# Kernel tuning notes

Hardware: AMD Instinct MI355X
Metric: run time of the kernel (lower is better)

The kernel has to match this reference:

```python
import jax, jax.numpy as jnp
import numpy as np

B, T, N, IN_DIM = 32, 12, 1024, 1
HID, EMB, K, HOR, OUT = 64, 16, 2, 12, 1


def setup_inputs() -> dict:
    key = jax.random.key(0)
    ks = jax.random.split(key, 12)
    s = 0.1
    return {
        "x": jax.random.normal(ks[0], (B, T, N, IN_DIM), jnp.float32),
        "E": jax.random.normal(ks[1], (N, EMB), jnp.float32),
        # layer 1: gate (z,r) and candidate pools; in = IN_DIM + HID
        "Wg1": jax.random.normal(ks[2], (EMB, K, IN_DIM + HID, 2 * HID), jnp.float32) * s,
        "bg1": jax.random.normal(ks[3], (EMB, 2 * HID), jnp.float32) * s,
        "Wc1": jax.random.normal(ks[4], (EMB, K, IN_DIM + HID, HID), jnp.float32) * s,
        "bc1": jax.random.normal(ks[5], (EMB, HID), jnp.float32) * s,
        # layer 2: in = HID + HID
        "Wg2": jax.random.normal(ks[6], (EMB, K, 2 * HID, 2 * HID), jnp.float32) * s,
        "bg2": jax.random.normal(ks[7], (EMB, 2 * HID), jnp.float32) * s,
        "Wc2": jax.random.normal(ks[8], (EMB, K, 2 * HID, HID), jnp.float32) * s,
        "bc2": jax.random.normal(ks[9], (EMB, HID), jnp.float32) * s,
        # Conv2d(1, HOR*OUT, kernel=(1, HID)) == per-node linear HID -> HOR*OUT
        "Wout": jax.random.normal(ks[10], (HOR * OUT, HID), jnp.float32) * s,
        "bout": jnp.zeros((HOR * OUT,), jnp.float32),
    }


def _supports(E):
    # adaptive adjacency from node embeddings + Chebyshev polynomial set
    A = jax.nn.softmax(jax.nn.relu(E @ E.T), axis=1)  # [N, N]
    sup = [jnp.eye(E.shape[0], dtype=E.dtype), A]
    for _ in range(K - 2):
        sup.append(2.0 * (A @ sup[-1]) - sup[-2])
    return jnp.stack(sup[:K])  # [K, N, N]


def _gconv(x, sup, E, Wp, bp):
    # x: [B, N, Ci]; per-node weights generated from embeddings
    xg = jnp.einsum('knm,bmc->bnkc', sup, x)          # [B, N, K, Ci]
    W = jnp.einsum('nd,dkio->nkio', E, Wp)            # [N, K, Ci, Co]
    b = E @ bp                                        # [N, Co]
    return jnp.einsum('bnki,nkio->bno', xg, W) + b


def _layer(xs, sup, E, Wg, bg, Wc, bc):
    # xs: [T, B, N, Ci]; adaptive graph-conv GRU scanned over time
    hid = Wc.shape[-1]

    def step(h, x_t):
        zr = jax.nn.sigmoid(_gconv(jnp.concatenate([x_t, h], -1), sup, E, Wg, bg))
        z, r = jnp.split(zr, 2, axis=-1)
        hc = jnp.tanh(_gconv(jnp.concatenate([x_t, z * h], -1), sup, E, Wc, bc))
        h_new = r * h + (1.0 - r) * hc
        return h_new, h_new

    h0 = jnp.zeros((xs.shape[1], xs.shape[2], hid), xs.dtype)
    _, hs = jax.lax.scan(step, h0, xs)
    return hs  # [T, B, N, hid]


def reference(x, E, Wg1, bg1, Wc1, bc1, Wg2, bg2, Wc2, bc2, Wout, bout):
    sup = _supports(E)
    xs = jnp.swapaxes(x, 0, 1)                        # [T, B, N, in]
    h1 = _layer(xs, sup, E, Wg1, bg1, Wc1, bc1)       # [T, B, N, HID]
    h2 = _layer(h1, sup, E, Wg2, bg2, Wc2, bc2)       # [T, B, N, HID]
    h_last = h2[-1]                                   # [B, N, HID]
    out = jnp.einsum('bnh,oh->bno', h_last, Wout) + bout  # [B, N, HOR*OUT]
    out = jnp.transpose(out, (0, 2, 1)).reshape(x.shape[0], HOR, OUT, N)
    return jnp.transpose(out, (0, 1, 3, 2))           # [B, HOR, N, OUT]
```

## Files before the change

kernel.cpp:

```cpp
#include <hip/hip_runtime.h>
#include <math.h>

#define NN 1024
#define BB 32
#define TTT 12
#define HH 64
#define DD 16

__device__ __forceinline__ float dot4f(const float4 v, const float* __restrict__ wv) {
    return v.x * wv[0] + v.y * wv[1] + v.z * wv[2] + v.w * wv[3];
}

__device__ __forceinline__ float sigmoidf_(float x) { return 1.0f / (1.0f + expf(-x)); }

__global__ __launch_bounds__(256) void compute_A_kernel(const float* __restrict__ E,
                                                        float* __restrict__ A) {
    int n = blockIdx.x;
    int tid = threadIdx.x;
    __shared__ float en[DD];
    __shared__ float red[256];
    if (tid < DD) en[tid] = E[n * DD + tid];
    __syncthreads();
    float s[4];
    float lmax = 0.0f;
    #pragma unroll
    for (int it = 0; it < 4; ++it) {
        int m = tid + it * 256;
        float acc = 0.0f;
        #pragma unroll
        for (int d = 0; d < DD; ++d) acc += en[d] * E[m * DD + d];
        acc = fmaxf(acc, 0.0f);
        s[it] = acc;
        lmax = fmaxf(lmax, acc);
    }
    red[tid] = lmax; __syncthreads();
    for (int st = 128; st > 0; st >>= 1) {
        if (tid < st) red[tid] = fmaxf(red[tid], red[tid + st]);
        __syncthreads();
    }
    float mx = red[0];
    __syncthreads();
    float lsum = 0.0f;
    #pragma unroll
    for (int it = 0; it < 4; ++it) { s[it] = expf(s[it] - mx); lsum += s[it]; }
    red[tid] = lsum; __syncthreads();
    for (int st = 128; st > 0; st >>= 1) {
        if (tid < st) red[tid] += red[tid + st];
        __syncthreads();
    }
    float inv = 1.0f / red[0];
    #pragma unroll
    for (int it = 0; it < 4; ++it) {
        int m = tid + it * 256;
        A[n * NN + m] = s[it] * inv;
    }
}

__global__ __launch_bounds__(256) void gen_w_f32_kernel(const float* __restrict__ E,
                                                        const float* __restrict__ Wp,
                                                        float* __restrict__ out,
                                                        int rowlen, int total) {
    int idx = blockIdx.x * 256 + threadIdx.x;
    if (idx >= total) return;
    int n = idx / rowlen;
    int j = idx - n * rowlen;
    const float* e = E + n * DD;
    float acc = 0.0f;
    #pragma unroll
    for (int d = 0; d < DD; ++d) acc += e[d] * Wp[d * rowlen + j];
    out[idx] = acc;
}

__global__ __launch_bounds__(256) void transpose_x_kernel(const float* __restrict__ x,
                                                          float* __restrict__ xTm) {
    int idx = blockIdx.x * 256 + threadIdx.x;
    int m = idx / (TTT * BB);
    int tb = idx - m * (TTT * BB);
    int t = tb >> 5;
    int b = tb & 31;
    xTm[idx] = x[(b * TTT + t) * NN + m];
}

__global__ __launch_bounds__(256) void diffuse_gemm(const float* __restrict__ A,
                                                    const float* __restrict__ S,
                                                    float* __restrict__ C, int cols) {
    __shared__ alignas(16) float As[16][68];
    __shared__ alignas(16) float Bs[16][64];
    const int tid = threadIdx.x;
    const int tx = tid & 15, ty = tid >> 4;
    const int rowbase = blockIdx.y * 64, colbase = blockIdx.x * 64;
    const int kl = tid & 15, r0 = (tid >> 4) * 4;
    const int ml = tid >> 6, cl = tid & 63;
    float pa[4], pb[4];
    #pragma unroll
    for (int r = 0; r < 4; ++r)
        pa[r] = A[(size_t)(rowbase + r0 + r) * NN + kl];
    #pragma unroll
    for (int mm = 0; mm < 4; ++mm)
        pb[mm] = S[(size_t)(ml + mm * 4) * cols + colbase + cl];
    float acc[4][4] = {};
    for (int kt = 0; kt < NN; kt += 16) {
        #pragma unroll
        for (int r = 0; r < 4; ++r) As[kl][r0 + r] = pa[r];
        #pragma unroll
        for (int mm = 0; mm < 4; ++mm) Bs[ml + mm * 4][cl] = pb[mm];
        __syncthreads();
        int kn = kt + 16;
        if (kn < NN) {
            #pragma unroll
            for (int r = 0; r < 4; ++r)
                pa[r] = A[(size_t)(rowbase + r0 + r) * NN + kn + kl];
            #pragma unroll
            for (int mm = 0; mm < 4; ++mm)
                pb[mm] = S[(size_t)(kn + ml + mm * 4) * cols + colbase + cl];
        }
        #pragma unroll
        for (int kk = 0; kk < 16; ++kk) {
            float4 a = *(const float4*)&As[kk][ty * 4];
            float4 b = *(const float4*)&Bs[kk][tx * 4];
            acc[0][0] += a.x * b.x; acc[0][1] += a.x * b.y; acc[0][2] += a.x * b.z; acc[0][3] += a.x * b.w;
            acc[1][0] += a.y * b.x; acc[1][1] += a.y * b.y; acc[1][2] += a.y * b.z; acc[1][3] += a.y * b.w;
            acc[2][0] += a.z * b.x; acc[2][1] += a.z * b.y; acc[2][2] += a.z * b.z; acc[2][3] += a.z * b.w;
            acc[3][0] += a.w * b.x; acc[3][1] += a.w * b.y; acc[3][2] += a.w * b.z; acc[3][3] += a.w * b.w;
        }
        __syncthreads();
    }
    #pragma unroll
    for (int i = 0; i < 4; ++i) {
        float4 v = make_float4(acc[i][0], acc[i][1], acc[i][2], acc[i][3]);
        *(float4*)&C[(size_t)(rowbase + ty * 4 + i) * cols + colbase + tx * 4] = v;
    }
}


__global__ __launch_bounds__(256) void l1_gate_fused(int t,
        const float* __restrict__ xTm, const float* __restrict__ AxA,
        const float* __restrict__ h1, const float* __restrict__ Ah1,
        const float* __restrict__ E, const float4* __restrict__ Wp4,
        const float* __restrict__ Bg,
        float* __restrict__ zh, float* __restrict__ rb) {
    int n = blockIdx.x, tid = threadIdx.x;
    __shared__ float en[DD];
    __shared__ alignas(16) float Wl[65 * 128];
    __shared__ alignas(16) float S0[BB * HH];
    __shared__ alignas(16) float S1[BB * HH];
    __shared__ float sx[BB], sax[BB];
    if (tid < DD) en[tid] = E[n * DD + tid];
    for (int i = tid; i < BB * HH; i += 256) {
        S0[i] = h1[(size_t)n * (BB * HH) + i];
        S1[i] = Ah1[(size_t)n * (BB * HH) + i];
    }
    if (tid < BB) sx[tid] = xTm[n * (TTT * BB) + t * BB + tid];
    else if (tid < 2 * BB) sax[tid - BB] = AxA[n * (TTT * BB) + t * BB + (tid - BB)];
    __syncthreads();
    const int o = tid & 63, bq = tid >> 6;
    float accA[8], accB[8];
    float biasA = Bg[n * 128 + o], biasB = Bg[n * 128 + 64 + o];
    #pragma unroll
    for (int j = 0; j < 8; ++j) { accA[j] = biasA; accB[j] = biasB; }
    for (int k = 0; k < 2; ++k) {
        for (int idx = tid; idx < 2080; idx += 256) {
            float4 a = make_float4(0.f, 0.f, 0.f, 0.f);
            #pragma unroll
            for (int d = 0; d < DD; ++d) {
                float ed = en[d];
                float4 w = Wp4[(size_t)d * 4160 + k * 2080 + idx];
                a.x += ed * w.x; a.y += ed * w.y; a.z += ed * w.z; a.w += ed * w.w;
            }
            *(float4*)&Wl[idx * 4] = a;
        }
        __syncthreads();
        const float* S = (k == 0) ? S0 : S1;
        float wxa = Wl[o], wxb = Wl[64 + o];
        #pragma unroll
        for (int j = 0; j < 8; ++j) {
            int b = bq * 8 + j;
            float xv = (k == 0) ? sx[b] : sax[b];
            accA[j] += xv * wxa; accB[j] += xv * wxb;
        }
        for (int i = 0; i < HH; i += 4) {
            float wa[4], wb[4];
            #pragma unroll
            for (int q = 0; q < 4; ++q) {
                int row = (1 + i + q) * 128;
                wa[q] = Wl[row + o]; wb[q] = Wl[row + 64 + o];
            }
            #pragma unroll
            for (int j = 0; j < 8; ++j) {
                int b = bq * 8 + j;
                float4 sv = *(const float4*)&S[b * HH + i];
                accA[j] += dot4f(sv, wa); accB[j] += dot4f(sv, wb);
            }
        }
        __syncthreads();
    }
    #pragma unroll
    for (int j = 0; j < 8; ++j) {
        int b = bq * 8 + j;
        float z = sigmoidf_(accA[j]);
        float r = sigmoidf_(accB[j]);
        zh[(size_t)n * (BB * HH) + b * HH + o] = z * S0[b * HH + o];
        rb[(size_t)n * (BB * HH) + b * HH + o] = r;
    }
}

__global__ __launch_bounds__(256) void l1_cand_fused(int t,
        const float* __restrict__ xTm, const float* __restrict__ AxA,
        const float* __restrict__ zhb, const float* __restrict__ azh,
        const float* __restrict__ E, const float4* __restrict__ Wp4,
        const float* __restrict__ Bc,
        const float* __restrict__ rb, float* __restrict__ h1) {
    int n = blockIdx.x, tid = threadIdx.x;
    __shared__ float en[DD];
    __shared__ alignas(16) float Wl[65 * 64];
    __shared__ alignas(16) float S0[BB * HH];
    __shared__ alignas(16) float S1[BB * HH];
    __shared__ float sx[BB], sax[BB];
    if (tid < DD) en[tid] = E[n * DD + tid];
    for (int i = tid; i < BB * HH; i += 256) {
        S0[i] = zhb[(size_t)n * (BB * HH) + i];
        S1[i] = azh[(size_t)n * (BB * HH) + i];
    }
    if (tid < BB) sx[tid] = xTm[n * (TTT * BB) + t * BB + tid];
    else if (tid < 2 * BB) sax[tid - BB] = AxA[n * (TTT * BB) + t * BB + (tid - BB)];
    __syncthreads();
    const int o = tid & 63, bq = tid >> 6;
    float acc[8];
    float bias = Bc[n * 64 + o];
    #pragma unroll
    for (int j = 0; j < 8; ++j) acc[j] = bias;
    for (int k = 0; k < 2; ++k) {
        for (int idx = tid; idx < 1040; idx += 256) {
            float4 a = make_float4(0.f, 0.f, 0.f, 0.f);
            #pragma unroll
            for (int d = 0; d < DD; ++d) {
                float ed = en[d];
                float4 w = Wp4[(size_t)d * 2080 + k * 1040 + idx];
                a.x += ed * w.x; a.y += ed * w.y; a.z += ed * w.z; a.w += ed * w.w;
            }
            *(float4*)&Wl[idx * 4] = a;
        }
        __syncthreads();
        const float* S = (k == 0) ? S0 : S1;
        float wx = Wl[o];
        #pragma unroll
        for (int j = 0; j < 8; ++j) {
            int b = bq * 8 + j;
            float xv = (k == 0) ? sx[b] : sax[b];
            acc[j] += xv * wx;
        }
        for (int i = 0; i < HH; i += 4) {
            float wa[4];
            #pragma unroll
            for (int q = 0; q < 4; ++q) wa[q] = Wl[(1 + i + q) * 64 + o];
            #pragma unroll
            for (int j = 0; j < 8; ++j) {
                int b = bq * 8 + j;
                float4 sv = *(const float4*)&S[b * HH + i];
                acc[j] += dot4f(sv, wa);
            }
        }
        __syncthreads();
    }
    #pragma unroll
    for (int j = 0; j < 8; ++j) {
        int b = bq * 8 + j;
        size_t idx = (size_t)n * (BB * HH) + b * HH + o;
        float hc = tanhf(acc[j]);
        float r = rb[idx];
        float hold = h1[idx];
        h1[idx] = r * hold + (1.0f - r) * hc;
    }
}

__global__ __launch_bounds__(256) void l2_gate_fused(
        const float* __restrict__ h1, const float* __restrict__ Ah1,
        const float* __restrict__ h2, const float* __restrict__ Ah2,
        const float* __restrict__ E, const float4* __restrict__ Wp4,
        const float* __restrict__ Bg,
        float* __restrict__ zh, float* __restrict__ rb) {
    int n = blockIdx.x, tid = threadIdx.x;
    __shared__ float en[DD];
    __shared__ alignas(16) float Wl[64 * 128];
    __shared__ alignas(16) float Sl[4][BB * HH];
    if (tid < DD) en[tid] = E[n * DD + tid];
    for (int i = tid; i < BB * HH; i += 256) {
        size_t base = (size_t)n * (BB * HH) + i;
        Sl[0][i] = h1[base]; Sl[1][i] = h2[base];
        Sl[2][i] = Ah1[base]; Sl[3][i] = Ah2[base];
    }
    __syncthreads();
    const int o = tid & 63, bq = tid >> 6;
    float accA[8], accB[8];
    float biasA = Bg[n * 128 + o], biasB = Bg[n * 128 + 64 + o];
    #pragma unroll
    for (int j = 0; j < 8; ++j) { accA[j] = biasA; accB[j] = biasB; }
    for (int p = 0; p < 4; ++p) {
        int k = p >> 1, half = p & 1;
        for (int idx = tid; idx < 2048; idx += 256) {
            float4 a = make_float4(0.f, 0.f, 0.f, 0.f);
            #pragma unroll
            for (int d = 0; d < DD; ++d) {
                float ed = en[d];
                float4 w = Wp4[(size_t)d * 8192 + k * 4096 + half * 2048 + idx];
                a.x += ed * w.x; a.y += ed * w.y; a.z += ed * w.z; a.w += ed * w.w;
            }
            *(float4*)&Wl[idx * 4] = a;
        }
        __syncthreads();
        const float* S = Sl[k * 2 + half];
        for (int i = 0; i < HH; i += 4) {
            float wa[4], wb[4];
            #pragma unroll
            for (int q = 0; q < 4; ++q) {
                int row = (i + q) * 128;
                wa[q] = Wl[row + o]; wb[q] = Wl[row + 64 + o];
            }
            #pragma unroll
            for (int j = 0; j < 8; ++j) {
                int b = bq * 8 + j;
                float4 sv = *(const float4*)&S[b * HH + i];
                accA[j] += dot4f(sv, wa); accB[j] += dot4f(sv, wb);
            }
        }
        __syncthreads();
    }
    #pragma unroll
    for (int j = 0; j < 8; ++j) {
        int b = bq * 8 + j;
        float z = sigmoidf_(accA[j]);
        float r = sigmoidf_(accB[j]);
        zh[(size_t)n * (BB * HH) + b * HH + o] = z * Sl[1][b * HH + o];
        rb[(size_t)n * (BB * HH) + b * HH + o] = r;
    }
}

__global__ __launch_bounds__(256) void l2_cand_fused(
        const float* __restrict__ h1, const float* __restrict__ Ah1,
        const float* __restrict__ zhb, const float* __restrict__ azh,
        const float* __restrict__ E, const float4* __restrict__ Wp4,
        const float* __restrict__ Bc,
        const float* __restrict__ rb, float* __restrict__ h2) {
    int n = blockIdx.x, tid = threadIdx.x;
    __shared__ float en[DD];
    __shared__ alignas(16) float Wl[64 * 64];
    __shared__ alignas(16) float Sl[4][BB * HH];
    if (tid < DD) en[tid] = E[n * DD + tid];
    for (int i = tid; i < BB * HH; i += 256) {
        size_t base = (size_t)n * (BB * HH) + i;
        Sl[0][i] = h1[base];  Sl[1][i] = zhb[base];
        Sl[2][i] = Ah1[base]; Sl[3][i] = azh[base];
    }
    __syncthreads();
    const int o = tid & 63, bq = tid >> 6;
    float acc[8];
    float bias = Bc[n * 64 + o];
    #pragma unroll
    for (int j = 0; j < 8; ++j) acc[j] = bias;
    for (int p = 0; p < 4; ++p) {
        int k = p >> 1, half = p & 1;
        for (int idx = tid; idx < 1024; idx += 256) {
            float4 a = make_float4(0.f, 0.f, 0.f, 0.f);
            #pragma unroll
            for (int d = 0; d < DD; ++d) {
                float ed = en[d];
                float4 w = Wp4[(size_t)d * 4096 + k * 2048 + half * 1024 + idx];
                a.x += ed * w.x; a.y += ed * w.y; a.z += ed * w.z; a.w += ed * w.w;
            }
            *(float4*)&Wl[idx * 4] = a;
        }
        __syncthreads();
        const float* S = Sl[k * 2 + half];
        for (int i = 0; i < HH; i += 4) {
            float wa[4];
            #pragma unroll
            for (int q = 0; q < 4; ++q) wa[q] = Wl[(i + q) * 64 + o];
            #pragma unroll
            for (int j = 0; j < 8; ++j) {
                int b = bq * 8 + j;
                float4 sv = *(const float4*)&S[b * HH + i];
                acc[j] += dot4f(sv, wa);
            }
        }
        __syncthreads();
    }
    #pragma unroll
    for (int j = 0; j < 8; ++j) {
        int b = bq * 8 + j;
        size_t idx = (size_t)n * (BB * HH) + b * HH + o;
        float hc = tanhf(acc[j]);
        float r = rb[idx];
        float hold = h2[idx];
        h2[idx] = r * hold + (1.0f - r) * hc;
    }
}

__global__ __launch_bounds__(384) void out_kernel(const float* __restrict__ h2,
                                                  const float* __restrict__ Wout,
                                                  const float* __restrict__ bout,
                                                  float* __restrict__ out) {
    int n = blockIdx.x;
    int tid = threadIdx.x;
    __shared__ float shh[BB * HH];
    __shared__ float sw[TTT * HH];
    __shared__ float sb[TTT];
    for (int i = tid; i < BB * HH; i += 384) shh[i] = h2[(size_t)n * (BB * HH) + i];
    for (int i = tid; i < TTT * HH; i += 384) sw[i] = Wout[i];
    if (tid < TTT) sb[tid] = bout[tid];
    __syncthreads();
    int b = tid & 31;
    int hor = tid >> 5;
    float acc = sb[hor];
    #pragma unroll
    for (int c = 0; c < HH; ++c) acc += shh[b * HH + c] * sw[hor * HH + c];
    out[(size_t)(b * TTT + hor) * NN + n] = acc;
}

__global__ void report_ws_kernel(float* out, float v) { out[0] = v; }

extern "C" void kernel_launch(void* const* d_in, const int* in_sizes, int n_in,
                              void* d_out, int out_size, void* d_ws, size_t ws_size,
                              hipStream_t stream) {
    const float* x    = (const float*)d_in[0];
    const float* E    = (const float*)d_in[1];
    const float* Wg1p = (const float*)d_in[2];
    const float* bg1p = (const float*)d_in[3];
    const float* Wc1p = (const float*)d_in[4];
    const float* bc1p = (const float*)d_in[5];
    const float* Wg2p = (const float*)d_in[6];
    const float* bg2p = (const float*)d_in[7];
    const float* Wc2p = (const float*)d_in[8];
    const float* bc2p = (const float*)d_in[9];
    const float* Wout = (const float*)d_in[10];
    const float* bout = (const float*)d_in[11];
    float* out = (float*)d_out;
    float* ws = (float*)d_ws;

    size_t off = 0;
    float* A_   = ws + off; off += (size_t)NN * NN;
    float* B1g  = ws + off; off += (size_t)NN * 128;
    float* B1c  = ws + off; off += (size_t)NN * 64;
    float* B2g  = ws + off; off += (size_t)NN * 128;
    float* B2c  = ws + off; off += (size_t)NN * 64;
    float* xTm  = ws + off; off += (size_t)NN * TTT * BB;
    float* AxA  = ws + off; off += (size_t)NN * TTT * BB;
    const size_t ST = (size_t)NN * BB * HH;
    float* h1   = ws + off; off += ST;
    float* h2   = ws + off; off += ST;
    float* Ah1  = ws + off; off += ST;
    float* Ah2  = ws + off; off += ST;
    float* Azh  = ws + off; off += ST;
    float* ZH   = ws + off; off += ST;
    float* Rb   = ws + off; off += ST;
    size_t need_bytes = off * sizeof(float);
    if (ws_size < need_bytes) {
        report_ws_kernel<<<1, 1, 0, stream>>>(out, (float)ws_size);
        return;
    }

    (void)hipMemsetAsync(h1, 0, ST * 4, stream);
    (void)hipMemsetAsync(h2, 0, ST * 4, stream);
    (void)hipMemsetAsync(Ah1, 0, ST * 4, stream);
    (void)hipMemsetAsync(Ah2, 0, ST * 4, stream);
    (void)hipMemsetAsync(Azh, 0, ST * 4, stream);

    compute_A_kernel<<<NN, 256, 0, stream>>>(E, A_);
    gen_w_f32_kernel<<<(131072 + 255) / 256, 256, 0, stream>>>(E, bg1p, B1g, 128, 131072);
    gen_w_f32_kernel<<<(65536 + 255) / 256, 256, 0, stream>>>(E, bc1p, B1c, 64, 65536);
    gen_w_f32_kernel<<<(131072 + 255) / 256, 256, 0, stream>>>(E, bg2p, B2g, 128, 131072);
    gen_w_f32_kernel<<<(65536 + 255) / 256, 256, 0, stream>>>(E, bc2p, B2c, 64, 65536);
    transpose_x_kernel<<<(NN * TTT * BB) / 256, 256, 0, stream>>>(x, xTm);
    diffuse_gemm<<<dim3((TTT * BB) / 64, NN / 64), 256, 0, stream>>>(A_, xTm, AxA, TTT * BB);

    const int COLS = BB * HH;
    dim3 gemmGrid(COLS / 64, NN / 64);

    for (int t = 0; t < TTT; ++t) {
        l1_gate_fused<<<NN, 256, 0, stream>>>(t, xTm, AxA, h1, Ah1,
                                              E, (const float4*)Wg1p, B1g, ZH, Rb);
        if (t > 0) diffuse_gemm<<<gemmGrid, 256, 0, stream>>>(A_, ZH, Azh, COLS);
        l1_cand_fused<<<NN, 256, 0, stream>>>(t, xTm, AxA, ZH, Azh,
                                              E, (const float4*)Wc1p, B1c, Rb, h1);
        diffuse_gemm<<<gemmGrid, 256, 0, stream>>>(A_, h1, Ah1, COLS);
        l2_gate_fused<<<NN, 256, 0, stream>>>(h1, Ah1, h2, Ah2,
                                              E, (const float4*)Wg2p, B2g, ZH, Rb);
        if (t > 0) diffuse_gemm<<<gemmGrid, 256, 0, stream>>>(A_, ZH, Azh, COLS);
        l2_cand_fused<<<NN, 256, 0, stream>>>(h1, Ah1, ZH, Azh,
                                              E, (const float4*)Wc2p, B2c, Rb, h2);
        if (t < TTT - 1) diffuse_gemm<<<gemmGrid, 256, 0, stream>>>(A_, h2, Ah2, COLS);
    }

    out_kernel<<<NN, 384, 0, stream>>>(h2, Wout, bout, out);
}
```

Baseline: 6.357 ms.

## Precompute layer-1 per-node weights once and double-buffer diffusion GEMM tiles

Measured after the change: 6.200 ms. 2.5% less time.

```diff
diff --git a/kernel.cpp b/kernel.cpp
--- a/kernel.cpp
+++ b/kernel.cpp
@@ -71,6 +71,25 @@
     out[idx] = acc;
 }
 
+__global__ __launch_bounds__(256) void gen_w4_kernel(const float* __restrict__ E,
+                                                     const float4* __restrict__ Wp4,
+                                                     float4* __restrict__ out4,
+                                                     int rowlen4, int total4) {
+    int idx = blockIdx.x * 256 + threadIdx.x;
+    if (idx >= total4) return;
+    int n = idx / rowlen4;
+    int j = idx - n * rowlen4;
+    const float* e = E + n * DD;
+    float4 acc = make_float4(0.f, 0.f, 0.f, 0.f);
+    #pragma unroll
+    for (int d = 0; d < DD; ++d) {
+        float ed = e[d];
+        float4 w = Wp4[(size_t)d * rowlen4 + j];
+        acc.x += ed * w.x; acc.y += ed * w.y; acc.z += ed * w.z; acc.w += ed * w.w;
+    }
+    out4[idx] = acc;
+}
+
 __global__ __launch_bounds__(256) void transpose_x_kernel(const float* __restrict__ x,
                                                           float* __restrict__ xTm) {
     int idx = blockIdx.x * 256 + threadIdx.x;
@@ -84,8 +103,8 @@
 __global__ __launch_bounds__(256) void diffuse_gemm(const float* __restrict__ A,
                                                     const float* __restrict__ S,
                                                     float* __restrict__ C, int cols) {
-    __shared__ alignas(16) float As[16][68];
-    __shared__ alignas(16) float Bs[16][64];
+    __shared__ alignas(16) float As[2][16][68];
+    __shared__ alignas(16) float Bs[2][16][64];
     const int tid = threadIdx.x;
     const int tx = tid & 15, ty = tid >> 4;
     const int rowbase = blockIdx.y * 64, colbase = blockIdx.x * 64;
@@ -98,13 +117,14 @@
     #pragma unroll
     for (int mm = 0; mm < 4; ++mm)
         pb[mm] = S[(size_t)(ml + mm * 4) * cols + colbase + cl];
+    #pragma unroll
+    for (int r = 0; r < 4; ++r) As[0][kl][r0 + r] = pa[r];
+    #pragma unroll
+    for (int mm = 0; mm < 4; ++mm) Bs[0][ml + mm * 4][cl] = pb[mm];
+    __syncthreads();
+    int cur = 0;
     float acc[4][4] = {};
     for (int kt = 0; kt < NN; kt += 16) {
-        #pragma unroll
-        for (int r = 0; r < 4; ++r) As[kl][r0 + r] = pa[r];
-        #pragma unroll
-        for (int mm = 0; mm < 4; ++mm) Bs[ml + mm * 4][cl] = pb[mm];
-        __syncthreads();
         int kn = kt + 16;
         if (kn < NN) {
             #pragma unroll
@@ -116,14 +136,22 @@
         }
         #pragma unroll
         for (int kk = 0; kk < 16; ++kk) {
-            float4 a = *(const float4*)&As[kk][ty * 4];
-            float4 b = *(const float4*)&Bs[kk][tx * 4];
+            float4 a = *(const float4*)&As[cur][kk][ty * 4];
+            float4 b = *(const float4*)&Bs[cur][kk][tx * 4];
             acc[0][0] += a.x * b.x; acc[0][1] += a.x * b.y; acc[0][2] += a.x * b.z; acc[0][3] += a.x * b.w;
             acc[1][0] += a.y * b.x; acc[1][1] += a.y * b.y; acc[1][2] += a.y * b.z; acc[1][3] += a.y * b.w;
             acc[2][0] += a.z * b.x; acc[2][1] += a.z * b.y; acc[2][2] += a.z * b.z; acc[2][3] += a.z * b.w;
             acc[3][0] += a.w * b.x; acc[3][1] += a.w * b.y; acc[3][2] += a.w * b.z; acc[3][3] += a.w * b.w;
         }
-        __syncthreads();
+        if (kn < NN) {
+            int nxt = cur ^ 1;
+            #pragma unroll
+            for (int r = 0; r < 4; ++r) As[nxt][kl][r0 + r] = pa[r];
+            #pragma unroll
+            for (int mm = 0; mm < 4; ++mm) Bs[nxt][ml + mm * 4][cl] = pb[mm];
+            __syncthreads();
+            cur = nxt;
+        }
     }
     #pragma unroll
     for (int i = 0; i < 4; ++i) {
@@ -133,134 +161,106 @@
 }
 
 
-__global__ __launch_bounds__(256) void l1_gate_fused(int t,
+__global__ __launch_bounds__(256) void l1_gate_kernel(int t,
         const float* __restrict__ xTm, const float* __restrict__ AxA,
         const float* __restrict__ h1, const float* __restrict__ Ah1,
-        const float* __restrict__ E, const float4* __restrict__ Wp4,
-        const float* __restrict__ Bg,
+        const float* __restrict__ Wg, const float* __restrict__ Bg,
         float* __restrict__ zh, float* __restrict__ rb) {
-    int n = blockIdx.x, tid = threadIdx.x;
-    __shared__ float en[DD];
-    __shared__ alignas(16) float Wl[65 * 128];
-    __shared__ alignas(16) float S0[BB * HH];
-    __shared__ alignas(16) float S1[BB * HH];
+    int n = blockIdx.x;
+    int tid = threadIdx.x;
+    __shared__ alignas(16) float sh[BB * HH];
+    __shared__ alignas(16) float sa[BB * HH];
     __shared__ float sx[BB], sax[BB];
-    if (tid < DD) en[tid] = E[n * DD + tid];
     for (int i = tid; i < BB * HH; i += 256) {
-        S0[i] = h1[(size_t)n * (BB * HH) + i];
-        S1[i] = Ah1[(size_t)n * (BB * HH) + i];
+        sh[i] = h1[(size_t)n * (BB * HH) + i];
+        sa[i] = Ah1[(size_t)n * (BB * HH) + i];
     }
     if (tid < BB) sx[tid] = xTm[n * (TTT * BB) + t * BB + tid];
     else if (tid < 2 * BB) sax[tid - BB] = AxA[n * (TTT * BB) + t * BB + (tid - BB)];
     __syncthreads();
-    const int o = tid & 63, bq = tid >> 6;
+    const int o = tid & 63;
+    const int bq = tid >> 6;
+    const float* W = Wg + (size_t)n * 16640;
     float accA[8], accB[8];
     float biasA = Bg[n * 128 + o], biasB = Bg[n * 128 + 64 + o];
-    #pragma unroll
-    for (int j = 0; j < 8; ++j) { accA[j] = biasA; accB[j] = biasB; }
-    for (int k = 0; k < 2; ++k) {
-        for (int idx = tid; idx < 2080; idx += 256) {
-            float4 a = make_float4(0.f, 0.f, 0.f, 0.f);
-            #pragma unroll
-            for (int d = 0; d < DD; ++d) {
-                float ed = en[d];
-                float4 w = Wp4[(size_t)d * 4160 + k * 2080 + idx];
-                a.x += ed * w.x; a.y += ed * w.y; a.z += ed * w.z; a.w += ed * w.w;
-            }
-            *(float4*)&Wl[idx * 4] = a;
-        }
-        __syncthreads();
-        const float* S = (k == 0) ? S0 : S1;
-        float wxa = Wl[o], wxb = Wl[64 + o];
+    float wxa0 = W[o], wxa1 = W[8320 + o];
+    float wxb0 = W[64 + o], wxb1 = W[8320 + 64 + o];
+    #pragma unroll
+    for (int j = 0; j < 8; ++j) {
+        int b = bq * 8 + j;
+        accA[j] = biasA + sx[b] * wxa0 + sax[b] * wxa1;
+        accB[j] = biasB + sx[b] * wxb0 + sax[b] * wxb1;
+    }
+    for (int i = 0; i < HH; i += 4) {
+        float w0a[4], w1a[4], w0b[4], w1b[4];
+        #pragma unroll
+        for (int q = 0; q < 4; ++q) {
+            int row = (1 + i + q) * 128;
+            w0a[q] = W[row + o];            w1a[q] = W[8320 + row + o];
+            w0b[q] = W[row + 64 + o];       w1b[q] = W[8320 + row + 64 + o];
+        }
         #pragma unroll
         for (int j = 0; j < 8; ++j) {
             int b = bq * 8 + j;
-            float xv = (k == 0) ? sx[b] : sax[b];
-            accA[j] += xv * wxa; accB[j] += xv * wxb;
-        }
-        for (int i = 0; i < HH; i += 4) {
-            float wa[4], wb[4];
-            #pragma unroll
-            for (int q = 0; q < 4; ++q) {
-                int row = (1 + i + q) * 128;
-                wa[q] = Wl[row + o]; wb[q] = Wl[row + 64 + o];
-            }
-            #pragma unroll
-            for (int j = 0; j < 8; ++j) {
-                int b = bq * 8 + j;
-                float4 sv = *(const float4*)&S[b * HH + i];
-                accA[j] += dot4f(sv, wa); accB[j] += dot4f(sv, wb);
-            }
-        }
-        __syncthreads();
+            float4 hv = *(const float4*)&sh[b * HH + i];
+            float4 av = *(const float4*)&sa[b * HH + i];
+            accA[j] += dot4f(hv, w0a) + dot4f(av, w1a);
+            accB[j] += dot4f(hv, w0b) + dot4f(av, w1b);
+        }
     }
     #pragma unroll
     for (int j = 0; j < 8; ++j) {
         int b = bq * 8 + j;
         float z = sigmoidf_(accA[j]);
         float r = sigmoidf_(accB[j]);
-        zh[(size_t)n * (BB * HH) + b * HH + o] = z * S0[b * HH + o];
+        zh[(size_t)n * (BB * HH) + b * HH + o] = z * sh[b * HH + o];
         rb[(size_t)n * (BB * HH) + b * HH + o] = r;
     }
 }
 
-__global__ __launch_bounds__(256) void l1_cand_fused(int t,
+__global__ __launch_bounds__(256) void l1_cand_kernel(int t,
         const float* __restrict__ xTm, const float* __restrict__ AxA,
         const float* __restrict__ zhb, const float* __restrict__ azh,
-        const float* __restrict__ E, const float4* __restrict__ Wp4,
-        const float* __restrict__ Bc,
+        const float* __restrict__ Wc, const float* __restrict__ Bc,
         const float* __restrict__ rb, float* __restrict__ h1) {
-    int n = blockIdx.x, tid = threadIdx.x;
-    __shared__ float en[DD];
-    __shared__ alignas(16) float Wl[65 * 64];
-    __shared__ alignas(16) float S0[BB * HH];
-    __shared__ alignas(16) float S1[BB * HH];
+    int n = blockIdx.x;
+    int tid = threadIdx.x;
+    __shared__ alignas(16) float sz[BB * HH];
+    __shared__ alignas(16) float saz[BB * HH];
     __shared__ float sx[BB], sax[BB];
-    if (tid < DD) en[tid] = E[n * DD + tid];
     for (int i = tid; i < BB * HH; i += 256) {
-        S0[i] = zhb[(size_t)n * (BB * HH) + i];
-        S1[i] = azh[(size_t)n * (BB * HH) + i];
+        sz[i] = zhb[(size_t)n * (BB * HH) + i];
+        saz[i] = azh[(size_t)n * (BB * HH) + i];
     }
     if (tid < BB) sx[tid] = xTm[n * (TTT * BB) + t * BB + tid];
     else if (tid < 2 * BB) sax[tid - BB] = AxA[n * (TTT * BB) + t * BB + (tid - BB)];
     __syncthreads();
-    const int o = tid & 63, bq = tid >> 6;
+    const int o = tid & 63;
+    const int bq = tid >> 6;
+    const float* W = Wc + (size_t)n * 8320;
     float acc[8];
     float bias = Bc[n * 64 + o];
-    #pragma unroll
-    for (int j = 0; j < 8; ++j) acc[j] = bias;
-    for (int k = 0; k < 2; ++k) {
-        for (int idx = tid; idx < 1040; idx += 256) {
-            float4 a = make_float4(0.f, 0.f, 0.f, 0.f);
-            #pragma unroll
-            for (int d = 0; d < DD; ++d) {
-                float ed = en[d];
-                float4 w = Wp4[(size_t)d * 2080 + k * 1040 + idx];
-                a.x += ed * w.x; a.y += ed * w.y; a.z += ed * w.z; a.w += ed * w.w;
-            }
-            *(float4*)&Wl[idx * 4] = a;
-        }
-        __syncthreads();
-        const float* S = (k == 0) ? S0 : S1;
-        float wx = Wl[o];
+    float wx0 = W[o], wx1 = W[4160 + o];
+    #pragma unroll
+    for (int j = 0; j < 8; ++j) {
+        int b = bq * 8 + j;
+        acc[j] = bias + sx[b] * wx0 + sax[b] * wx1;
+    }
+    for (int i = 0; i < HH; i += 4) {
+        float w0[4], w1[4];
+        #pragma unroll
+        for (int q = 0; q < 4; ++q) {
+            int row = (1 + i + q) * 64;
+            w0[q] = W[row + o];
+            w1[q] = W[4160 + row + o];
+        }
         #pragma unroll
         for (int j = 0; j < 8; ++j) {
             int b = bq * 8 + j;
-            float xv = (k == 0) ? sx[b] : sax[b];
-            acc[j] += xv * wx;
-        }
-        for (int i = 0; i < HH; i += 4) {
-            float wa[4];
-            #pragma unroll
-            for (int q = 0; q < 4; ++q) wa[q] = Wl[(1 + i + q) * 64 + o];
-            #pragma unroll
-            for (int j = 0; j < 8; ++j) {
-                int b = bq * 8 + j;
-                float4 sv = *(const float4*)&S[b * HH + i];
-                acc[j] += dot4f(sv, wa);
-            }
-        }
-        __syncthreads();
+            float4 zv = *(const float4*)&sz[b * HH + i];
+            float4 av = *(const float4*)&saz[b * HH + i];
+            acc[j] += dot4f(zv, w0) + dot4f(av, w1);
+        }
     }
     #pragma unroll
     for (int j = 0; j < 8; ++j) {
@@ -272,6 +272,7 @@
         h1[idx] = r * hold + (1.0f - r) * hc;
     }
 }
+
 
 __global__ __launch_bounds__(256) void l2_gate_fused(
         const float* __restrict__ h1, const float* __restrict__ Ah1,
@@ -374,7 +375,7 @@
         for (int i = 0; i < HH; i += 4) {
             float wa[4];
             #pragma unroll
-            for (int q = 0; q < 4; ++q) wa[q] = Wl[(i + q) * 64 + o];
+            for (int qq = 0; qq < 4; ++qq) wa[qq] = Wl[(i + qq) * 64 + o];
             #pragma unroll
             for (int j = 0; j < 8; ++j) {
                 int b = bq * 8 + j;
@@ -452,6 +453,8 @@
     float* Azh  = ws + off; off += ST;
     float* ZH   = ws + off; off += ST;
     float* Rb   = ws + off; off += ST;
+    float* W1G  = ws + off; off += (size_t)NN * 16640;
+    float* W1C  = ws + off; off += (size_t)NN * 8320;
     size_t need_bytes = off * sizeof(float);
     if (ws_size < need_bytes) {
         report_ws_kernel<<<1, 1, 0, stream>>>(out, (float)ws_size);
@@ -471,16 +474,18 @@
     gen_w_f32_kernel<<<(65536 + 255) / 256, 256, 0, stream>>>(E, bc2p, B2c, 64, 65536);
     transpose_x_kernel<<<(NN * TTT * BB) / 256, 256, 0, stream>>>(x, xTm);
     diffuse_gemm<<<dim3((TTT * BB) / 64, NN / 64), 256, 0, stream>>>(A_, xTm, AxA, TTT * BB);
+    gen_w4_kernel<<<(4259840 + 255) / 256, 256, 0, stream>>>(
+        E, (const float4*)Wg1p, (float4*)W1G, 4160, 4259840);
+    gen_w4_kernel<<<(2129920 + 255) / 256, 256, 0, stream>>>(
+        E, (const float4*)Wc1p, (float4*)W1C, 2080, 2129920);
 
     const int COLS = BB * HH;
     dim3 gemmGrid(COLS / 64, NN / 64);
 
     for (int t = 0; t < TTT; ++t) {
-        l1_gate_fused<<<NN, 256, 0, stream>>>(t, xTm, AxA, h1, Ah1,
-                                              E, (const float4*)Wg1p, B1g, ZH, Rb);
+        l1_gate_kernel<<<NN, 256, 0, stream>>>(t, xTm, AxA, h1, Ah1, W1G, B1g, ZH, Rb);
         if (t > 0) diffuse_gemm<<<gemmGrid, 256, 0, stream>>>(A_, ZH, Azh, COLS);
-        l1_cand_fused<<<NN, 256, 0, stream>>>(t, xTm, AxA, ZH, Azh,
-                                              E, (const float4*)Wc1p, B1c, Rb, h1);
+        l1_cand_kernel<<<NN, 256, 0, stream>>>(t, xTm, AxA, ZH, Azh, W1C, B1c, Rb, h1);
         diffuse_gemm<<<gemmGrid, 256, 0, stream>>>(A_, h1, Ah1, COLS);
         l2_gate_fused<<<NN, 256, 0, stream>>>(h1, Ah1, h2, Ah2,
                                               E, (const float4*)Wg2p, B2g, ZH, Rb);
```
